# Optimization experiments

Measured on AMD Instinct MI355X. Metric: run time of the kernel, lower is better.

The kernel has to match this reference:

```python
import jax, jax.numpy as jnp
import numpy as np

N_NODES = 100000
N_EDGES = 1600000
C = 256            # in_channels == out_channels
NUM_BUNDLES = 64
BUNDLE_DIM = 2
NUM_GRAPHS = 128
BN_EPS = 1e-5


def setup_inputs() -> dict:
    key = jax.random.key(0)
    ks = jax.random.split(key, 12)
    x = jax.random.normal(ks[0], (N_NODES, C), dtype=jnp.float32)
    edge_index = jax.random.randint(ks[1], (2, N_EDGES), 0, N_NODES, dtype=jnp.int64)
    batch = jnp.sort(jax.random.randint(ks[2], (N_NODES,), 0, NUM_GRAPHS, dtype=jnp.int64))
    s = 0.05
    # struct_enc MLP: Linear(C, 2*NB) -> GELU -> Linear(2*NB, NB)
    se_w1 = jax.random.normal(ks[3], (C, 2 * NUM_BUNDLES), dtype=jnp.float32) * s
    se_b1 = jnp.zeros((2 * NUM_BUNDLES,), dtype=jnp.float32)
    se_w2 = jax.random.normal(ks[4], (2 * NUM_BUNDLES, NUM_BUNDLES), dtype=jnp.float32) * s
    se_b2 = jnp.zeros((NUM_BUNDLES,), dtype=jnp.float32)
    # LimConv.lin: Linear(C, C)
    lin_w = jax.random.normal(ks[5], (C, C), dtype=jnp.float32) * s
    lin_b = jnp.zeros((C,), dtype=jnp.float32)
    # BatchNorm1d affine params
    bn_gamma = jnp.ones((C,), dtype=jnp.float32)
    bn_beta = jnp.zeros((C,), dtype=jnp.float32)
    return {"x": x, "edge_index": edge_index, "batch": batch,
            "se_w1": se_w1, "se_b1": se_b1, "se_w2": se_w2, "se_b2": se_b2,
            "lin_w": lin_w, "lin_b": lin_b, "bn_gamma": bn_gamma, "bn_beta": bn_beta}


def _lim_layer(x, batch, se_w1, se_b1, se_w2, se_b2, lin_w, lin_b, bn_gamma, bn_beta):
    n = x.shape[0]
    # vector field: [N, NB, 2, fiber]
    vf = x.reshape(n, NUM_BUNDLES, BUNDLE_DIM, -1)
    # struct_enc MLP -> per-bundle angle (tanh-squashed), euler map to SO(2)
    h1 = jax.nn.gelu(x @ se_w1 + se_b1, approximate=False)
    ang = jnp.tanh(h1 @ se_w2 + se_b2)          # [N, NB]
    c, s = jnp.cos(ang), jnp.sin(ang)
    # R[n,b] = [[c,-s],[s,c]]  -> [N, NB, 2, 2]
    rot = jnp.stack([jnp.stack([c, -s], axis=-1),
                     jnp.stack([s, c], axis=-1)], axis=-2)
    # rotate fibers
    vf = jnp.einsum('nbij,nbjf->nbif', rot, vf)
    h = vf.reshape(n, C) @ lin_w + lin_b
    # global mean pool over graphs, then broadcast back to nodes
    sums = jax.ops.segment_sum(h, batch, num_segments=NUM_GRAPHS)
    cnts = jax.ops.segment_sum(jnp.ones((n,), h.dtype), batch, num_segments=NUM_GRAPHS)
    hmean = sums / jnp.maximum(cnts, 1.0)[:, None]
    h = hmean[batch]
    # inverse rotation (R^T)
    vf = h.reshape(n, NUM_BUNDLES, BUNDLE_DIM, -1)
    vf = jnp.einsum('nbji,nbjf->nbif', rot, vf)
    h = vf.reshape(n, C)
    # residual (dim_in == dim_out)
    h = x + h
    # dropout p=0 / eval -> identity. BatchNorm1d with batch statistics.
    mu = jnp.mean(h, axis=0)
    var = jnp.var(h, axis=0)
    h = (h - mu) * jax.lax.rsqrt(var + BN_EPS) * bn_gamma + bn_beta
    return h


def reference(x, edge_index, batch, se_w1, se_b1, se_w2, se_b2, lin_w, lin_b, bn_gamma, bn_beta):
    # edge_index is unused when num_gnn == 0 (struct_enc is an MLP), as in the source.
    del edge_index
    return _lim_layer(x, batch, se_w1, se_b1, se_w2, se_b2, lin_w, lin_b, bn_gamma, bn_beta)
```

## Files before the change

### kernel.cpp

```cpp
#include <hip/hip_runtime.h>
#include <hip/hip_bf16.h>
#include <math.h>

#define N_NODES 100000
#define C 256
#define NB 64
#define H1D 128
#define NG 128
#define GS 257
#define BN_EPS 1e-5f

#define BLKN 64
#define NBLK1 ((N_NODES + BLKN - 1) / BLKN)

#define OFF_GSUMS 0
#define OFF_BNSUM (NG * GS)
#define OFF_BNSQ  (OFF_BNSUM + 256)
#define ZERO_FLOATS (OFF_BNSQ + 256)
#define OFF_HMEAN ZERO_FLOATS
#define OFF_WT1   (OFF_HMEAN + NG * C)
#define OFF_WT2   (OFF_WT1 + 16896)
#define OFF_CS    (OFF_WT2 + 4352)
#define OFF_SN    (OFF_CS + N_NODES * NB / 2)

#define WT1_LD 264
#define WT2_LD 136

typedef __attribute__((ext_vector_type(8))) short bf16x8;
typedef __attribute__((ext_vector_type(4))) float f32x4;

__device__ __forceinline__ float bf2f(__hip_bfloat16 h) { return __bfloat162float(h); }

__global__ __launch_bounds__(256)
void k0_prep(const float* __restrict__ W1, const float* __restrict__ W2,
             __hip_bfloat16* __restrict__ Wt1, __hip_bfloat16* __restrict__ Wt2)
{
    const int t0 = threadIdx.x + blockIdx.x * 256;
    const int stride = gridDim.x * 256;
    for (int i = t0; i < 128 * 256; i += stride) {
        int n = i >> 8, k = i & 255;
        Wt1[n * WT1_LD + k] = __float2bfloat16(W1[k * 128 + n]);
    }
    for (int i = t0; i < 64 * 128; i += stride) {
        int n = i >> 7, k = i & 127;
        Wt2[n * WT2_LD + k] = __float2bfloat16(W2[k * 64 + n]);
    }
}

__global__ __launch_bounds__(256, 2)
void k1_angles_rot_pool(const float* __restrict__ x,
                        const int* __restrict__ batch,
                        const __hip_bfloat16* __restrict__ Wt1g,
                        const float* __restrict__ b1,
                        const __hip_bfloat16* __restrict__ Wt2g,
                        const float* __restrict__ b2,
                        float* __restrict__ gsums,
                        __hip_bfloat16* __restrict__ csg,
                        __hip_bfloat16* __restrict__ sng)
{
    __shared__ __hip_bfloat16 xs[BLKN][264];
    __shared__ __hip_bfloat16 h1s[BLKN][136];
    __shared__ __hip_bfloat16 csb[BLKN][72];
    __shared__ __hip_bfloat16 snb[BLKN][72];

    const int t = threadIdx.x;
    const int w = t >> 6;
    const int l = t & 63;
    const int lo = l & 15, quad = l >> 4;
    const int n0 = blockIdx.x * BLKN;
    const int nrem = min(BLKN, N_NODES - n0);

    #pragma unroll
    for (int m = 0; m < 16; ++m) {
        int idx = t + m * 256;
        int r = idx >> 6, c4 = (idx & 63) * 4;
        float4 v;
        if (n0 + r < N_NODES) v = *(const float4*)(x + (size_t)(n0 + r) * C + c4);
        else { v.x = v.y = v.z = v.w = 0.f; }
        __hip_bfloat16* p = &xs[r][c4];
        p[0] = __float2bfloat16(v.x); p[1] = __float2bfloat16(v.y);
        p[2] = __float2bfloat16(v.z); p[3] = __float2bfloat16(v.w);
    }

    bf16x8 bfr[2][8];
    #pragma unroll
    for (int nt = 0; nt < 2; ++nt) {
        const short* base = (const short*)Wt1g + (w * 32 + nt * 16 + lo) * WT1_LD + quad * 8;
        #pragma unroll
        for (int k = 0; k < 8; ++k) bfr[nt][k] = *(const bf16x8*)(base + k * 32);
    }
    bf16x8 b2f[4][4];
    #pragma unroll
    for (int nt = 0; nt < 4; ++nt) {
        const short* base = (const short*)Wt2g + (nt * 16 + lo) * WT2_LD + quad * 8;
        #pragma unroll
        for (int k = 0; k < 4; ++k) b2f[nt][k] = *(const bf16x8*)(base + k * 32);
    }
    __syncthreads();

    f32x4 acc1[4][2];
    #pragma unroll
    for (int mt = 0; mt < 4; ++mt) { acc1[mt][0] = (f32x4)0.f; acc1[mt][1] = (f32x4)0.f; }
    #pragma unroll
    for (int mt = 0; mt < 4; ++mt) {
        #pragma unroll
        for (int k = 0; k < 8; ++k) {
            bf16x8 afr = *(const bf16x8*)&xs[mt * 16 + lo][k * 32 + quad * 8];
            acc1[mt][0] = __builtin_amdgcn_mfma_f32_16x16x32_bf16(afr, bfr[0][k], acc1[mt][0], 0, 0, 0);
            acc1[mt][1] = __builtin_amdgcn_mfma_f32_16x16x32_bf16(afr, bfr[1][k], acc1[mt][1], 0, 0, 0);
        }
    }
    #pragma unroll
    for (int nt = 0; nt < 2; ++nt) {
        const float bb = b1[w * 32 + nt * 16 + lo];
        #pragma unroll
        for (int mt = 0; mt < 4; ++mt) {
            #pragma unroll
            for (int r = 0; r < 4; ++r) {
                float v = acc1[mt][nt][r] + bb;
                v = 0.5f * v * (1.0f + erff(v * 0.70710678118654752f));
                h1s[mt * 16 + quad * 4 + r][w * 32 + nt * 16 + lo] = __float2bfloat16(v);
            }
        }
    }
    __syncthreads();

    f32x4 acc2[4];
    #pragma unroll
    for (int nt = 0; nt < 4; ++nt) acc2[nt] = (f32x4)0.f;
    #pragma unroll
    for (int k = 0; k < 4; ++k) {
        bf16x8 afr = *(const bf16x8*)&h1s[w * 16 + lo][k * 32 + quad * 8];
        #pragma unroll
        for (int nt = 0; nt < 4; ++nt)
            acc2[nt] = __builtin_amdgcn_mfma_f32_16x16x32_bf16(afr, b2f[nt][k], acc2[nt], 0, 0, 0);
    }
    #pragma unroll
    for (int nt = 0; nt < 4; ++nt) {
        const float bb = b2[nt * 16 + lo];
        #pragma unroll
        for (int r = 0; r < 4; ++r) {
            float a = tanhf(acc2[nt][r] + bb);
            float sv, cv;
            sincosf(a, &sv, &cv);
            int row = w * 16 + quad * 4 + r;
            csb[row][nt * 16 + lo] = __float2bfloat16(cv);
            snb[row][nt * 16 + lo] = __float2bfloat16(sv);
        }
    }
    __syncthreads();

    #pragma unroll
    for (int m = 0; m < 8; ++m) {
        int idx = t + m * 256;
        int row = idx >> 5;
        int c2 = (idx & 31) * 2;
        if (n0 + row < N_NODES) {
            *(unsigned int*)(csg + (size_t)(n0 + row) * NB + c2) = *(const unsigned int*)&csb[row][c2];
            *(unsigned int*)(sng + (size_t)(n0 + row) * NB + c2) = *(const unsigned int*)&snb[row][c2];
        }
    }

    {
        const int b = t >> 2;
        const int idx = t & 3;
        const int i2 = idx >> 1;
        const int f = idx & 1;
        float racc = 0.f;
        int rcnt = 0;
        int gprev = batch[n0];
        for (int r = 0; r < nrem; ++r) {
            const int g = batch[n0 + r];
            if (g != gprev) {
                atomicAdd(&gsums[gprev * GS + t], racc);
                if (t == 0) atomicAdd(&gsums[gprev * GS + 256], (float)rcnt);
                racc = 0.f; rcnt = 0; gprev = g;
            }
            const float x0 = bf2f(xs[r][4 * b + f]);
            const float x1 = bf2f(xs[r][4 * b + 2 + f]);
            const float cb = bf2f(csb[r][b]);
            const float sb = bf2f(snb[r][b]);
            const float xr = (i2 == 0) ? (cb * x0 - sb * x1) : (sb * x0 + cb * x1);
            racc += xr;
            rcnt++;
        }
        atomicAdd(&gsums[gprev * GS + t], racc);
        if (t == 0) atomicAdd(&gsums[gprev * GS + 256], (float)rcnt);
    }
}

__global__ __launch_bounds__(256)
void k2_hmean(const float* __restrict__ gsums, const float* __restrict__ lin_w,
              const float* __restrict__ lin_b, float* __restrict__ hmean)
{
    __shared__ float gs[C];
    __shared__ float cnt_sh;
    const int g = blockIdx.x;
    const int t = threadIdx.x;
    gs[t] = gsums[g * GS + t];
    if (t == 0) cnt_sh = gsums[g * GS + 256];
    __syncthreads();
    float a0 = 0.f, a1 = 0.f, a2 = 0.f, a3 = 0.f;
    #pragma unroll 4
    for (int k = 0; k < C; k += 4) {
        a0 += gs[k + 0] * lin_w[(size_t)(k + 0) * C + t];
        a1 += gs[k + 1] * lin_w[(size_t)(k + 1) * C + t];
        a2 += gs[k + 2] * lin_w[(size_t)(k + 2) * C + t];
        a3 += gs[k + 3] * lin_w[(size_t)(k + 3) * C + t];
    }
    const float cnt = cnt_sh;
    hmean[g * C + t] = (cnt > 0.f) ? ((a0 + a1 + a2 + a3) / cnt + lin_b[t]) : 0.f;
}

__global__ __launch_bounds__(256, 4)
void k3_inverse_resid(const float* __restrict__ x,
                      const int* __restrict__ batch,
                      const __hip_bfloat16* __restrict__ csg,
                      const __hip_bfloat16* __restrict__ sng,
                      const float* __restrict__ hmean,
                      float* __restrict__ out,
                      float* __restrict__ bnsum, float* __restrict__ bnsq)
{
    __shared__ float rs[4][C];
    __shared__ float rq[4][C];
    const int t = threadIdx.x;
    const int s = t >> 6;
    const int cg = t & 63;
    float bs0 = 0.f, bs1 = 0.f, bs2 = 0.f, bs3 = 0.f;
    float bq0 = 0.f, bq1 = 0.f, bq2 = 0.f, bq3 = 0.f;

    for (int base = blockIdx.x * 4; base < N_NODES; base += gridDim.x * 4) {
        const int n = base + s;
        if (n < N_NODES) {
            const int g = batch[n];
            const float4 hm = *(const float4*)(hmean + (size_t)g * C + cg * 4);
            const float cv = bf2f(csg[(size_t)n * NB + cg]);
            const float sv = bf2f(sng[(size_t)n * NB + cg]);
            const float4 xv = *(const float4*)(x + (size_t)n * C + cg * 4);
            float4 o;
            o.x = xv.x + cv * hm.x + sv * hm.z;
            o.y = xv.y + cv * hm.y + sv * hm.w;
            o.z = xv.z - sv * hm.x + cv * hm.z;
            o.w = xv.w - sv * hm.y + cv * hm.w;
            *(float4*)(out + (size_t)n * C + cg * 4) = o;
            bs0 += o.x; bs1 += o.y; bs2 += o.z; bs3 += o.w;
            bq0 += o.x * o.x; bq1 += o.y * o.y; bq2 += o.z * o.z; bq3 += o.w * o.w;
        }
    }
    rs[s][cg * 4 + 0] = bs0; rs[s][cg * 4 + 1] = bs1;
    rs[s][cg * 4 + 2] = bs2; rs[s][cg * 4 + 3] = bs3;
    rq[s][cg * 4 + 0] = bq0; rq[s][cg * 4 + 1] = bq1;
    rq[s][cg * 4 + 2] = bq2; rq[s][cg * 4 + 3] = bq3;
    __syncthreads();
    atomicAdd(&bnsum[t], rs[0][t] + rs[1][t] + rs[2][t] + rs[3][t]);
    atomicAdd(&bnsq[t],  rq[0][t] + rq[1][t] + rq[2][t] + rq[3][t]);
}

__global__ __launch_bounds__(256)
void k4_bn(float* __restrict__ out, const float* __restrict__ bnsum,
           const float* __restrict__ bnsq, const float* __restrict__ gamma,
           const float* __restrict__ beta)
{
    __shared__ float mul_s[C], add_s[C];
    const int t = threadIdx.x;
    {
        const float inv_n = 1.0f / (float)N_NODES;
        const float mu = bnsum[t] * inv_n;
        const float var = bnsq[t] * inv_n - mu * mu;
        const float inv = rsqrtf(var + BN_EPS);
        const float m = gamma[t] * inv;
        mul_s[t] = m;
        add_s[t] = beta[t] - mu * m;
    }
    __syncthreads();
    float4* o4 = (float4*)out;
    const size_t total = (size_t)N_NODES * C / 4;
    for (size_t i = (size_t)blockIdx.x * 256 + t; i < total;
         i += (size_t)gridDim.x * 256) {
        float4 v = o4[i];
        const int c0 = ((int)(i & 63)) * 4;
        v.x = v.x * mul_s[c0 + 0] + add_s[c0 + 0];
        v.y = v.y * mul_s[c0 + 1] + add_s[c0 + 1];
        v.z = v.z * mul_s[c0 + 2] + add_s[c0 + 2];
        v.w = v.w * mul_s[c0 + 3] + add_s[c0 + 3];
        o4[i] = v;
    }
}

extern "C" void kernel_launch(void* const* d_in, const int* in_sizes, int n_in,
                              void* d_out, int out_size, void* d_ws, size_t ws_size,
                              hipStream_t stream)
{
    const float* x      = (const float*)d_in[0];
    const int* batch    = (const int*)d_in[2];
    const float* W1     = (const float*)d_in[3];
    const float* b1     = (const float*)d_in[4];
    const float* W2     = (const float*)d_in[5];
    const float* b2     = (const float*)d_in[6];
    const float* lin_w  = (const float*)d_in[7];
    const float* lin_b  = (const float*)d_in[8];
    const float* gamma  = (const float*)d_in[9];
    const float* beta   = (const float*)d_in[10];

    float* ws    = (float*)d_ws;
    float* gsums = ws + OFF_GSUMS;
    float* bnsum = ws + OFF_BNSUM;
    float* bnsq  = ws + OFF_BNSQ;
    float* hmean = ws + OFF_HMEAN;
    __hip_bfloat16* Wt1 = (__hip_bfloat16*)(ws + OFF_WT1);
    __hip_bfloat16* Wt2 = (__hip_bfloat16*)(ws + OFF_WT2);
    __hip_bfloat16* csg = (__hip_bfloat16*)(ws + OFF_CS);
    __hip_bfloat16* sng = (__hip_bfloat16*)(ws + OFF_SN);
    float* out   = (float*)d_out;

    hipMemsetAsync(gsums, 0, ZERO_FLOATS * sizeof(float), stream);

    k0_prep<<<32, 256, 0, stream>>>(W1, W2, Wt1, Wt2);
    k1_angles_rot_pool<<<NBLK1, 256, 0, stream>>>(x, batch, Wt1, b1, Wt2, b2,
                                                  gsums, csg, sng);
    k2_hmean<<<NG, 256, 0, stream>>>(gsums, lin_w, lin_b, hmean);
    k3_inverse_resid<<<512, 256, 0, stream>>>(x, batch, csg, sng, hmean, out,
                                              bnsum, bnsq);
    k4_bn<<<2048, 256, 0, stream>>>(out, bnsum, bnsq, gamma, beta);
}
```

Baseline: 362.3 us.

## Interleave cos/sin storage, alias k1 shared memory, and cache batch ids

Packs cos and sin into one interleaved bf16 array so k3 reads one 32-bit word per bundle instead of two scattered halves. k1 reuses the h1 shared buffer for the cos/sin tile, which shrinks LDS enough to raise the occupancy hint to 3 blocks. It also stages batch ids in shared memory and vectorises the bf16 stores and loads in the pooling loop. k3's grid is doubled. The extra barrier and the float count with a padded loop add small overheads.

```diff
diff --git a/kernel.cpp b/kernel.cpp
--- a/kernel.cpp
+++ b/kernel.cpp
@@ -20,14 +20,15 @@
 #define OFF_HMEAN ZERO_FLOATS
 #define OFF_WT1   (OFF_HMEAN + NG * C)
 #define OFF_WT2   (OFF_WT1 + 16896)
-#define OFF_CS    (OFF_WT2 + 4352)
-#define OFF_SN    (OFF_CS + N_NODES * NB / 2)
+#define OFF_CSN   (OFF_WT2 + 4352)
 
 #define WT1_LD 264
 #define WT2_LD 136
 
 typedef __attribute__((ext_vector_type(8))) short bf16x8;
 typedef __attribute__((ext_vector_type(4))) float f32x4;
+
+struct __align__(8) bf4 { __hip_bfloat16 x, y, z, w; };
 
 __device__ __forceinline__ float bf2f(__hip_bfloat16 h) { return __bfloat162float(h); }
 
@@ -47,7 +48,7 @@
     }
 }
 
-__global__ __launch_bounds__(256, 2)
+__global__ __launch_bounds__(256, 3)
 void k1_angles_rot_pool(const float* __restrict__ x,
                         const int* __restrict__ batch,
                         const __hip_bfloat16* __restrict__ Wt1g,
@@ -55,13 +56,13 @@
                         const __hip_bfloat16* __restrict__ Wt2g,
                         const float* __restrict__ b2,
                         float* __restrict__ gsums,
-                        __hip_bfloat16* __restrict__ csg,
-                        __hip_bfloat16* __restrict__ sng)
+                        __hip_bfloat16* __restrict__ csng)
 {
     __shared__ __hip_bfloat16 xs[BLKN][264];
-    __shared__ __hip_bfloat16 h1s[BLKN][136];
-    __shared__ __hip_bfloat16 csb[BLKN][72];
-    __shared__ __hip_bfloat16 snb[BLKN][72];
+    __shared__ char sm_u[BLKN * WT2_LD * 2];
+    __shared__ int gsh[BLKN];
+    auto h1s = (__hip_bfloat16 (*)[WT2_LD])sm_u;
+    auto csn = (__hip_bfloat16 (*)[132])sm_u;
 
     const int t = threadIdx.x;
     const int w = t >> 6;
@@ -77,10 +78,12 @@
         float4 v;
         if (n0 + r < N_NODES) v = *(const float4*)(x + (size_t)(n0 + r) * C + c4);
         else { v.x = v.y = v.z = v.w = 0.f; }
-        __hip_bfloat16* p = &xs[r][c4];
-        p[0] = __float2bfloat16(v.x); p[1] = __float2bfloat16(v.y);
-        p[2] = __float2bfloat16(v.z); p[3] = __float2bfloat16(v.w);
-    }
+        bf4 pk;
+        pk.x = __float2bfloat16(v.x); pk.y = __float2bfloat16(v.y);
+        pk.z = __float2bfloat16(v.z); pk.w = __float2bfloat16(v.w);
+        *(bf4*)&xs[r][c4] = pk;
+    }
+    if (t < BLKN) gsh[t] = batch[min(n0 + t, N_NODES - 1)];
 
     bf16x8 bfr[2][8];
     #pragma unroll
@@ -135,6 +138,8 @@
         for (int nt = 0; nt < 4; ++nt)
             acc2[nt] = __builtin_amdgcn_mfma_f32_16x16x32_bf16(afr, b2f[nt][k], acc2[nt], 0, 0, 0);
     }
+    __syncthreads();
+
     #pragma unroll
     for (int nt = 0; nt < 4; ++nt) {
         const float bb = b2[nt * 16 + lo];
@@ -143,49 +148,50 @@
             float a = tanhf(acc2[nt][r] + bb);
             float sv, cv;
             sincosf(a, &sv, &cv);
-            int row = w * 16 + quad * 4 + r;
-            csb[row][nt * 16 + lo] = __float2bfloat16(cv);
-            snb[row][nt * 16 + lo] = __float2bfloat16(sv);
-        }
-    }
-    __syncthreads();
-
-    #pragma unroll
-    for (int m = 0; m < 8; ++m) {
+            union { unsigned int u; __hip_bfloat16 h[2]; } p;
+            p.h[0] = __float2bfloat16(cv);
+            p.h[1] = __float2bfloat16(sv);
+            *(unsigned int*)&csn[w * 16 + quad * 4 + r][2 * (nt * 16 + lo)] = p.u;
+        }
+    }
+    __syncthreads();
+
+    #pragma unroll
+    for (int m = 0; m < 16; ++m) {
         int idx = t + m * 256;
-        int row = idx >> 5;
-        int c2 = (idx & 31) * 2;
-        if (n0 + row < N_NODES) {
-            *(unsigned int*)(csg + (size_t)(n0 + row) * NB + c2) = *(const unsigned int*)&csb[row][c2];
-            *(unsigned int*)(sng + (size_t)(n0 + row) * NB + c2) = *(const unsigned int*)&snb[row][c2];
-        }
+        int row = idx >> 6;
+        int d = (idx & 63) * 2;
+        if (n0 + row < N_NODES)
+            *(unsigned int*)(csng + (size_t)(n0 + row) * 128 + d) = *(const unsigned int*)&csn[row][d];
     }
 
     {
         const int b = t >> 2;
-        const int idx = t & 3;
-        const int i2 = idx >> 1;
-        const int f = idx & 1;
-        float racc = 0.f;
-        int rcnt = 0;
-        int gprev = batch[n0];
-        for (int r = 0; r < nrem; ++r) {
-            const int g = batch[n0 + r];
+        const int idx2 = t & 3;
+        const int i2 = idx2 >> 1;
+        const int f = idx2 & 1;
+        float racc = 0.f, rcnt = 0.f;
+        int gprev = gsh[0];
+        #pragma unroll 16
+        for (int r = 0; r < BLKN; ++r) {
+            const int g = gsh[r];
             if (g != gprev) {
                 atomicAdd(&gsums[gprev * GS + t], racc);
-                if (t == 0) atomicAdd(&gsums[gprev * GS + 256], (float)rcnt);
-                racc = 0.f; rcnt = 0; gprev = g;
+                if (t == 0) atomicAdd(&gsums[gprev * GS + 256], rcnt);
+                racc = 0.f; rcnt = 0.f; gprev = g;
             }
-            const float x0 = bf2f(xs[r][4 * b + f]);
-            const float x1 = bf2f(xs[r][4 * b + 2 + f]);
-            const float cb = bf2f(csb[r][b]);
-            const float sb = bf2f(snb[r][b]);
-            const float xr = (i2 == 0) ? (cb * x0 - sb * x1) : (sb * x0 + cb * x1);
-            racc += xr;
-            rcnt++;
+            bf4 xq = *(const bf4*)&xs[r][4 * b];
+            union { unsigned int u; __hip_bfloat16 h[2]; } cs;
+            cs.u = *(const unsigned int*)&csn[r][2 * b];
+            const float x0 = f ? bf2f(xq.y) : bf2f(xq.x);
+            const float x1 = f ? bf2f(xq.w) : bf2f(xq.z);
+            const float cb = bf2f(cs.h[0]);
+            const float sb = bf2f(cs.h[1]);
+            racc += (i2 == 0) ? (cb * x0 - sb * x1) : (sb * x0 + cb * x1);
+            rcnt += (r < nrem) ? 1.f : 0.f;
         }
         atomicAdd(&gsums[gprev * GS + t], racc);
-        if (t == 0) atomicAdd(&gsums[gprev * GS + 256], (float)rcnt);
+        if (t == 0) atomicAdd(&gsums[gprev * GS + 256], rcnt);
     }
 }
 
@@ -215,8 +221,7 @@
 __global__ __launch_bounds__(256, 4)
 void k3_inverse_resid(const float* __restrict__ x,
                       const int* __restrict__ batch,
-                      const __hip_bfloat16* __restrict__ csg,
-                      const __hip_bfloat16* __restrict__ sng,
+                      const __hip_bfloat16* __restrict__ csng,
                       const float* __restrict__ hmean,
                       float* __restrict__ out,
                       float* __restrict__ bnsum, float* __restrict__ bnsq)
@@ -234,8 +239,10 @@
         if (n < N_NODES) {
             const int g = batch[n];
             const float4 hm = *(const float4*)(hmean + (size_t)g * C + cg * 4);
-            const float cv = bf2f(csg[(size_t)n * NB + cg]);
-            const float sv = bf2f(sng[(size_t)n * NB + cg]);
+            union { unsigned int u; __hip_bfloat16 h[2]; } cs;
+            cs.u = *(const unsigned int*)(csng + (size_t)n * 128 + cg * 2);
+            const float cv = bf2f(cs.h[0]);
+            const float sv = bf2f(cs.h[1]);
             const float4 xv = *(const float4*)(x + (size_t)n * C + cg * 4);
             float4 o;
             o.x = xv.x + cv * hm.x + sv * hm.z;
@@ -307,19 +314,18 @@
     float* bnsum = ws + OFF_BNSUM;
     float* bnsq  = ws + OFF_BNSQ;
     float* hmean = ws + OFF_HMEAN;
-    __hip_bfloat16* Wt1 = (__hip_bfloat16*)(ws + OFF_WT1);
-    __hip_bfloat16* Wt2 = (__hip_bfloat16*)(ws + OFF_WT2);
-    __hip_bfloat16* csg = (__hip_bfloat16*)(ws + OFF_CS);
-    __hip_bfloat16* sng = (__hip_bfloat16*)(ws + OFF_SN);
+    __hip_bfloat16* Wt1  = (__hip_bfloat16*)(ws + OFF_WT1);
+    __hip_bfloat16* Wt2  = (__hip_bfloat16*)(ws + OFF_WT2);
+    __hip_bfloat16* csng = (__hip_bfloat16*)(ws + OFF_CSN);
     float* out   = (float*)d_out;
 
     hipMemsetAsync(gsums, 0, ZERO_FLOATS * sizeof(float), stream);
 
     k0_prep<<<32, 256, 0, stream>>>(W1, W2, Wt1, Wt2);
     k1_angles_rot_pool<<<NBLK1, 256, 0, stream>>>(x, batch, Wt1, b1, Wt2, b2,
-                                                  gsums, csg, sng);
+                                                  gsums, csng);
     k2_hmean<<<NG, 256, 0, stream>>>(gsums, lin_w, lin_b, hmean);
-    k3_inverse_resid<<<512, 256, 0, stream>>>(x, batch, csg, sng, hmean, out,
-                                              bnsum, bnsq);
+    k3_inverse_resid<<<1024, 256, 0, stream>>>(x, batch, csng, hmean, out,
+                                               bnsum, bnsq);
     k4_bn<<<2048, 256, 0, stream>>>(out, bnsum, bnsq, gamma, beta);
 }
```

After: 394.8 us. 9.0% more time.
